# Performance work log

Measured on AMD Instinct MI355X. Metric: run time of the kernel, lower is better.

## Reference

```python
import math
import jax, jax.numpy as jnp
import numpy as np

B, S, E = 4, 2048, 768
H, D = 12, 64
LOCAL_H, GLOBAL_H = 8, 4
WINDOW_BASE, MIN_W, MAX_W = 128, 32, 512
GLOBAL_RATIO = 0.1
MASK_VALUE = -1e9


def setup_inputs() -> dict:
    key = jax.random.key(0)
    k1, k2, k3 = jax.random.split(key, 3)
    return {
        "x": jax.random.normal(k1, (B, S, E), dtype=jnp.float32),
        "w_attn": jax.random.normal(k2, (E, 3 * E), dtype=jnp.float32) * 0.02,
        "b_attn": jnp.zeros((3 * E,), dtype=jnp.float32),
        "w_proj": jax.random.normal(k3, (E, E), dtype=jnp.float32) * 0.02,
        "b_proj": jnp.zeros((E,), dtype=jnp.float32),
    }


def _masks(seq_len: int):
    # dynamic window (adaptive): base * sqrt(S/base), clamped
    w = int(WINDOW_BASE * math.sqrt(seq_len / WINDOW_BASE))
    w = max(MIN_W, min(w, MAX_W))
    half = w // 2
    i = jnp.arange(seq_len)[:, None]
    j = jnp.arange(seq_len)[None, :]
    # local: window band then causal override -> allowed iff i-half <= j <= i
    local_allowed = (j >= i - half) & (j <= i)
    local_mask = jnp.where(local_allowed, 0.0, MASK_VALUE).astype(jnp.float32)
    # global: columns at linspace positions allowed for all rows, plus full causal
    n_glob = max(1, int(seq_len * GLOBAL_RATIO))
    gpos = jnp.linspace(0.0, seq_len - 1, n_glob).astype(jnp.int32)
    is_gcol = jnp.zeros((seq_len,), dtype=bool).at[gpos].set(True)
    global_allowed = (j <= i) | is_gcol[None, :]
    global_mask = jnp.where(global_allowed, 0.0, MASK_VALUE).astype(jnp.float32)
    return local_mask, global_mask


def _attend(q, k, v, mask):
    # q,k,v: [B,h,S,D]; mask: [S,S]
    scale = 1.0 / math.sqrt(q.shape[-1])
    scores = jnp.einsum("bhqd,bhkd->bhqk", q, k) * scale + mask[None, None]
    w = jax.nn.softmax(scores, axis=-1)
    return jnp.einsum("bhqk,bhkd->bhqd", w, v)


def reference(x, w_attn, b_attn, w_proj, b_proj):
    b, s, _ = x.shape
    qkv = x @ w_attn + b_attn                       # [B,S,3E]
    q, k, v = jnp.split(qkv, 3, axis=-1)
    def heads(t):
        return t.reshape(b, s, H, D).transpose(0, 2, 1, 3)  # [B,H,S,D]
    q, k, v = heads(q), heads(k), heads(v)
    local_mask, global_mask = _masks(s)
    local_out = _attend(q[:, :LOCAL_H], k[:, :LOCAL_H], v[:, :LOCAL_H], local_mask)
    global_out = _attend(q[:, LOCAL_H:], k[:, LOCAL_H:], v[:, LOCAL_H:], global_mask)
    attn = jnp.concatenate([local_out, global_out], axis=1)  # heads 0..7 local, 8..11 global
    attn = attn.transpose(0, 2, 1, 3).reshape(b, s, E)
    return attn @ w_proj + b_proj
```

## Files before the change

kernel.cpp:

```cpp
#include <hip/hip_runtime.h>
#include <stdint.h>


#define NH 12
#define SQ 2048

typedef __bf16 bf16x8 __attribute__((ext_vector_type(8)));
typedef float f32x4 __attribute__((ext_vector_type(4)));

#define GLOAD_LDS16(g, l)                                                      \
  __builtin_amdgcn_global_load_lds(                                            \
      (__attribute__((address_space(1))) void*)(g),                            \
      (__attribute__((address_space(3))) void*)(l), 16, 0, 0)

__device__ __forceinline__ unsigned short bfbits(float f) {
  __bf16 h = (__bf16)f;
  return *(unsigned short*)&h;
}

__global__ __launch_bounds__(256) void prep(
    const float* __restrict__ x, unsigned short* __restrict__ xb,
    const float* __restrict__ w_attn, unsigned short* __restrict__ wattnT,
    const float* __restrict__ w_proj, unsigned short* __restrict__ wprojT) {
  const int bid = blockIdx.x, t = threadIdx.x;
  if (bid < 512) {
    const int n4 = 8192 * 768 / 4;
    for (int i = bid * 256 + t; i < n4; i += 512 * 256) {
      float4 v = ((const float4*)x)[i];
      ((ushort4*)xb)[i] = make_ushort4(bfbits(v.x), bfbits(v.y), bfbits(v.z), bfbits(v.w));
    }
    return;
  }
  __shared__ float tile[32][33];
  const float* in; unsigned short* out; int K, N, tl;
  if (bid < 512 + 72 * 24) { in = w_attn; out = wattnT; K = 768; N = 2304; tl = bid - 512; }
  else                     { in = w_proj; out = wprojT; K = 768; N = 768;  tl = bid - 512 - 72 * 24; }
  const int tpr = N / 32;
  const int n0 = (tl % tpr) * 32, k0 = (tl / tpr) * 32;
  const int tx = t & 31, ty = t >> 5;
  for (int r = ty; r < 32; r += 8) tile[r][tx] = in[(size_t)(k0 + r) * N + n0 + tx];
  __syncthreads();
  for (int r = ty; r < 32; r += 8) out[(size_t)(n0 + r) * K + k0 + tx] = bfbits(tile[tx][r]);
}

__global__ __launch_bounds__(256) void vprep(const unsigned short* __restrict__ QKV,
                                             const unsigned short* __restrict__ Vtb,
                                             unsigned short* __restrict__ Kg,
                                             unsigned short* __restrict__ VgT,
                                             int* __restrict__ gidx) {
  const int g = blockIdx.x, t = threadIdx.x;
  const int bh = g >> 3, y = g & 7;
  const int b = bh >> 2, h = 8 + (bh & 3);
  const int bh48 = b * NH + h;
  if (g == 0) {
    int c = t;
    gidx[c] = (c < 203) ? (int)((double)c * (2047.0 / 203.0)) : ((c == 203) ? 2047 : -1);
  }
  {
    int c = t, ch = y;
    int col = (c < 203) ? (int)((double)c * (2047.0 / 203.0)) : ((c == 203) ? 2047 : -1);
    uint4 v = {0u, 0u, 0u, 0u};
    if (col >= 0) v = *(const uint4*)&QKV[(size_t)(b * SQ + col) * 2304 + 768 + h * 64 + ch * 8];
    *(uint4*)&Kg[((size_t)bh * 256 + c) * 64 + ch * 8] = v;
  }
  {
    int d = t >> 2;
    int cb = (t & 3) * 64 + y * 8;
    for (int cc = 0; cc < 8; ++cc) {
      int c = cb + cc;
      int col = (c < 203) ? (int)((double)c * (2047.0 / 203.0)) : ((c == 203) ? 2047 : -1);
      unsigned short v = 0;
      if (col >= 0) v = Vtb[(size_t)bh48 * 131072 + (size_t)d * 2048 + col];
      VgT[((size_t)bh * 64 + d) * 256 + c] = v;
    }
  }
}

__device__ __forceinline__ void gemm_mainloop(
    const unsigned short* __restrict__ A, const unsigned short* __restrict__ BT,
    int m0, int n0, int tid,
    unsigned short* As, unsigned short* Bs,
    f32x4 acc[4][4]) {
  const int lane = tid & 63, wave = tid >> 6;
  const int wm = wave >> 1, wn = wave & 1;
  const int ln = lane & 15, quad = lane >> 4, ln7 = lane & 7;
  const int srow = tid >> 3;
  const int scol = ((tid & 7) ^ (srow & 7)) * 8;
  const int sbase = wave * 512;

#pragma unroll
  for (int mi = 0; mi < 4; ++mi)
#pragma unroll
    for (int ni = 0; ni < 4; ++ni) acc[mi][ni] = (f32x4){0.f, 0.f, 0.f, 0.f};

  auto stage = [&](int kt, int buf) {
    const int k0 = kt * 64;
    const int bo = buf * 8192;
#pragma unroll
    for (int rr = 0; rr < 4; ++rr) {
      GLOAD_LDS16(A  + (size_t)(m0 + rr * 32 + srow) * 768 + k0 + scol,
                  &As[bo + rr * 2048 + sbase]);
      GLOAD_LDS16(BT + (size_t)(n0 + rr * 32 + srow) * 768 + k0 + scol,
                  &Bs[bo + rr * 2048 + sbase]);
    }
  };

  stage(0, 0);
  int buf = 0;
  for (int kt = 0; kt < 12; ++kt) {
    if (kt < 11) {
      stage(kt + 1, buf ^ 1);
      asm volatile("s_waitcnt vmcnt(8)" ::: "memory");
    } else {
      asm volatile("s_waitcnt vmcnt(0)" ::: "memory");
    }
    __builtin_amdgcn_sched_barrier(0);
    __builtin_amdgcn_s_barrier();
    const int bo = buf * 8192;
#pragma unroll
    for (int kh = 0; kh < 2; ++kh) {
      const int sk = ((kh * 4 + quad) ^ ln7) * 8;
      bf16x8 aF[4], bF[4];
#pragma unroll
      for (int mi = 0; mi < 4; ++mi)
        aF[mi] = *(const bf16x8*)&As[bo + (wm * 64 + mi * 16 + ln) * 64 + sk];
#pragma unroll
      for (int ni = 0; ni < 4; ++ni)
        bF[ni] = *(const bf16x8*)&Bs[bo + (wn * 64 + ni * 16 + ln) * 64 + sk];
#pragma unroll
      for (int mi = 0; mi < 4; ++mi)
#pragma unroll
        for (int ni = 0; ni < 4; ++ni)
          acc[mi][ni] = __builtin_amdgcn_mfma_f32_16x16x32_bf16(aF[mi], bF[ni], acc[mi][ni], 0, 0, 0);
    }
    asm volatile("s_waitcnt lgkmcnt(0)" ::: "memory");
    __builtin_amdgcn_sched_barrier(0);
    __builtin_amdgcn_s_barrier();
    buf ^= 1;
  }
}

__global__ __launch_bounds__(256, 2) void qkv_gemm(
    const unsigned short* __restrict__ Xb, const unsigned short* __restrict__ WT,
    const float* __restrict__ bias, unsigned short* __restrict__ Out,
    unsigned short* __restrict__ Vtb) {
  __shared__ __attribute__((aligned(16))) unsigned short As[2 * 128 * 64];
  __shared__ __attribute__((aligned(16))) unsigned short Bs[2 * 128 * 64];
  f32x4 acc[4][4];
  const int wg = (blockIdx.x & 7) * 144 + (blockIdx.x >> 3);
  const int m0 = (wg / 18) * 128, n0 = (wg % 18) * 128;
  const int tid = threadIdx.x;
  gemm_mainloop(Xb, WT, m0, n0, tid, As, Bs, acc);
  const int lane = tid & 63, wave = tid >> 6;
  const int wm = wave >> 1, wn = wave & 1, ln = lane & 15, quad = lane >> 4;
  if (n0 < 1536) {
#pragma unroll
    for (int mi = 0; mi < 4; ++mi)
#pragma unroll
      for (int ni = 0; ni < 4; ++ni) {
        int n = n0 + wn * 64 + ni * 16 + ln;
        float bs = bias[n];
#pragma unroll
        for (int rg = 0; rg < 4; ++rg) {
          int m = m0 + wm * 64 + mi * 16 + quad * 4 + rg;
          Out[(size_t)m * 2304 + n] = bfbits(acc[mi][ni][rg] + bs);
        }
      }
  } else {
    const int bb = m0 >> 11;
    const int key0 = (m0 & 2047) + wm * 64;
#pragma unroll
    for (int ni = 0; ni < 4; ++ni) {
      int e = (n0 - 1536) + wn * 64 + ni * 16 + ln;
      int h = e >> 6, d = e & 63;
      float bs = bias[1536 + e];
      size_t rowb = (size_t)(bb * NH + h) * 131072 + (size_t)d * 2048;
#pragma unroll
      for (int mi = 0; mi < 4; ++mi) {
        int key = key0 + mi * 16 + quad * 4;
        unsigned int w0 = (unsigned int)bfbits(acc[mi][ni][0] + bs) |
                          ((unsigned int)bfbits(acc[mi][ni][1] + bs) << 16);
        unsigned int w1 = (unsigned int)bfbits(acc[mi][ni][2] + bs) |
                          ((unsigned int)bfbits(acc[mi][ni][3] + bs) << 16);
        *(unsigned int*)&Vtb[rowb + key]     = w0;
        *(unsigned int*)&Vtb[rowb + key + 2] = w1;
      }
    }
  }
}

__global__ __launch_bounds__(256, 2) void proj_gemm(
    const unsigned short* __restrict__ Ab, const unsigned short* __restrict__ WT,
    const float* __restrict__ bias, float* __restrict__ Out) {
  __shared__ __attribute__((aligned(16))) unsigned short As[2 * 128 * 64];
  __shared__ __attribute__((aligned(16))) unsigned short Bs[2 * 128 * 64];
  f32x4 acc[4][4];
  const int wg = (blockIdx.x & 7) * 48 + (blockIdx.x >> 3);
  const int m0 = (wg / 6) * 128, n0 = (wg % 6) * 128;
  const int tid = threadIdx.x;
  gemm_mainloop(Ab, WT, m0, n0, tid, As, Bs, acc);
  const int lane = tid & 63, wave = tid >> 6;
  const int wm = wave >> 1, wn = wave & 1, ln = lane & 15, quad = lane >> 4;
#pragma unroll
  for (int mi = 0; mi < 4; ++mi)
#pragma unroll
    for (int ni = 0; ni < 4; ++ni)
#pragma unroll
      for (int rg = 0; rg < 4; ++rg) {
        int m = m0 + wm * 64 + mi * 16 + quad * 4 + rg;
        int n = n0 + wn * 64 + ni * 16 + ln;
        Out[(size_t)m * 768 + n] = acc[mi][ni][rg] + bias[n];
      }
}

__global__ __launch_bounds__(256, 4) void attn_kernel(
    const unsigned short* __restrict__ QKV,
    const unsigned short* __restrict__ Vtb,
    const unsigned short* __restrict__ Kg, const unsigned short* __restrict__ VgT,
    const int* __restrict__ gidx,
    unsigned short* __restrict__ AOut,
    unsigned short* __restrict__ Opart,
    float* __restrict__ Lpart) {
  __shared__ __attribute__((aligned(16))) unsigned short Ks[64 * 64];
  __shared__ __attribute__((aligned(16))) unsigned short Vs[64 * 64];
  __shared__ __attribute__((aligned(16))) unsigned short Ps[64 * 64];

  const int gid = blockIdx.x;
  int b, h, qb, vt0, vt1;
  bool multi = false;
  if (gid < 1536) {
    int bh = gid / 96, rem = gid % 96;
    b = bh >> 2; h = 8 + (bh & 3);
    int part;
    if (rem < 4)       { qb = rem;                               part = 0; }
    else if (rem < 20) { int z = rem - 4;  qb = 4 + (z >> 1);    part = z & 1; }
    else if (rem < 44) { int z = rem - 20; int q = z / 3; qb = 12 + q; part = z - 3 * q; }
    else if (rem < 76) { int z = rem - 44; qb = 20 + (z >> 2);   part = z & 3; }
    else               { int z = rem - 76; int q = z / 5; qb = 28 + q; part = z - 5 * q; }
    vt0 = part * 8;
    vt1 = min(vt0 + 8, qb + 5);
    multi = (qb >= 4);
  } else {
    int lid = gid - 1536;
    int bh = lid >> 5; b = bh >> 3; h = bh & 7; qb = lid & 31;
    vt0 = ((qb > 4) ? qb - 4 : 0) + 4;
    vt1 = qb + 5;
  }
  const int qb0 = qb * 64;
  const bool is_local = (h < 8);
  const int tid = threadIdx.x, lane = tid & 63, wave = tid >> 6;
  const int ln = lane & 15, quad = lane >> 4;
  const int bh48 = b * NH + h;
  const int bhg = (b << 2) | (h & 3);

  const size_t qoff = (size_t)(b * SQ + qb0 + wave * 16 + ln) * 2304 + h * 64;
  bf16x8 qA0 = *(const bf16x8*)&QKV[qoff + quad * 8];
  bf16x8 qA1 = *(const bf16x8*)&QKV[qoff + 32 + quad * 8];

  bf16x8 onesF;
#pragma unroll
  for (int z = 0; z < 8; ++z) onesF[z] = (__bf16)1.0f;

  f32x4 o[4];
  f32x4 ls = (f32x4){0.f, 0.f, 0.f, 0.f};
#pragma unroll
  for (int dt = 0; dt < 4; ++dt) o[dt] = (f32x4){0.f, 0.f, 0.f, 0.f};

  const int irow = qb0 + wave * 16 + quad * 4;
  const int iw = qb0 + wave * 16;
  const int sr = tid >> 3, sch = tid & 7;
  const int ssw = (sch ^ (sr & 7)) * 8;
  const int s0k = (quad ^ (ln & 7)) * 8;
  const int s1k = ((quad + 4) ^ (ln & 7)) * 8;
  const int lnh = ln >> 3, ln7 = ln & 7;

  const float S2 = 0.125f * 1.44269504f, B2 = 8.0f * 1.44269504f;

  uint4 pk0, pk1, pv0, pv1;
  auto issue_load = [&](int vt) {
    if (vt >= 4) {
      const int kstart = (vt - 4) * 64;
      const size_t ko = (size_t)(b * SQ + kstart + sr) * 2304 + 768 + h * 64 + sch * 8;
      pk0 = *(const uint4*)&QKV[ko];
      pk1 = *(const uint4*)&QKV[ko + (size_t)32 * 2304];
      const size_t vo = (size_t)bh48 * 131072 + (size_t)sr * 2048 + kstart + sch * 8;
      pv0 = *(const uint4*)&Vtb[vo];
      pv1 = *(const uint4*)&Vtb[vo + 32 * 2048];
    } else {
      const int kg0 = vt * 64;
      pk0 = *(const uint4*)&Kg[((size_t)bhg * 256 + kg0 + sr) * 64 + sch * 8];
      pk1 = *(const uint4*)&Kg[((size_t)bhg * 256 + kg0 + 32 + sr) * 64 + sch * 8];
      pv0 = *(const uint4*)&VgT[((size_t)bhg * 64 + sr) * 256 + kg0 + sch * 8];
      pv1 = *(const uint4*)&VgT[((size_t)bhg * 64 + 32 + sr) * 256 + kg0 + sch * 8];
    }
  };
  issue_load(vt0);

  for (int vt = vt0; vt < vt1; ++vt) {
    const bool gph = (vt < 4);
    __syncthreads();
    *(uint4*)&Ks[sr * 64 + ssw]        = pk0;
    *(uint4*)&Ks[(32 + sr) * 64 + ssw] = pk1;
    *(uint4*)&Vs[sr * 64 + ssw]        = pv0;
    *(uint4*)&Vs[(32 + sr) * 64 + ssw] = pv1;
    __syncthreads();
    if (vt + 1 < vt1) issue_load(vt + 1);

    const int kstart = (vt - 4) * 64;
    const int kg0 = vt * 64;
    float sc[4][4];
    const bool full = !gph && (kstart + 63 <= iw) && (!is_local || kstart >= iw - 241);
#pragma unroll
    for (int nt = 0; nt < 4; ++nt) {
      bf16x8 kF0 = *(const bf16x8*)&Ks[(nt * 16 + ln) * 64 + s0k];
      bf16x8 kF1 = *(const bf16x8*)&Ks[(nt * 16 + ln) * 64 + s1k];
      f32x4 c = (f32x4){0.f, 0.f, 0.f, 0.f};
      c = __builtin_amdgcn_mfma_f32_16x16x32_bf16(qA0, kF0, c, 0, 0, 0);
      c = __builtin_amdgcn_mfma_f32_16x16x32_bf16(qA1, kF1, c, 0, 0, 0);
      if (full) {
#pragma unroll
        for (int rg = 0; rg < 4; ++rg) sc[nt][rg] = c[rg] * S2 - B2;
      } else if (!gph) {
        int j = kstart + nt * 16 + ln;
#pragma unroll
        for (int rg = 0; rg < 4; ++rg) {
          int i = irow + rg;
          bool ok = is_local ? (j >= i - 256 && j <= i) : (j <= i);
          sc[nt][rg] = ok ? (c[rg] * S2 - B2) : -1e9f;
        }
      } else {
        int jg = gidx[kg0 + nt * 16 + ln];
#pragma unroll
        for (int rg = 0; rg < 4; ++rg) {
          bool ok = jg > (irow + rg);
          sc[nt][rg] = ok ? (c[rg] * S2 - B2) : -1e9f;
        }
      }
    }

    __bf16* P = (__bf16*)Ps;
#pragma unroll
    for (int rg = 0; rg < 4; ++rg) {
      int prow = wave * 16 + quad * 4 + rg;
      int pbase = prow * 64 + ln7;
      int pr7 = prow & 7;
#pragma unroll
      for (int nt = 0; nt < 4; ++nt)
        P[pbase + (((nt * 2 + lnh) ^ pr7) << 3)] = (__bf16)exp2f(sc[nt][rg]);
    }
    bf16x8 pF0 = *(const bf16x8*)&Ps[(wave * 16 + ln) * 64 + s0k];
    bf16x8 pF1 = *(const bf16x8*)&Ps[(wave * 16 + ln) * 64 + s1k];
    ls = __builtin_amdgcn_mfma_f32_16x16x32_bf16(pF0, onesF, ls, 0, 0, 0);
    ls = __builtin_amdgcn_mfma_f32_16x16x32_bf16(pF1, onesF, ls, 0, 0, 0);
#pragma unroll
    for (int dt = 0; dt < 4; ++dt) {
      bf16x8 vF0 = *(const bf16x8*)&Vs[(dt * 16 + ln) * 64 + s0k];
      bf16x8 vF1 = *(const bf16x8*)&Vs[(dt * 16 + ln) * 64 + s1k];
      o[dt] = __builtin_amdgcn_mfma_f32_16x16x32_bf16(pF0, vF0, o[dt], 0, 0, 0);
      o[dt] = __builtin_amdgcn_mfma_f32_16x16x32_bf16(pF1, vF1, o[dt], 0, 0, 0);
    }
  }

  if (gid >= 1536 || !multi) {
#pragma unroll
    for (int dt = 0; dt < 4; ++dt)
#pragma unroll
      for (int rg = 0; rg < 4; ++rg) {
        int row = b * SQ + qb0 + wave * 16 + quad * 4 + rg;
        int e = h * 64 + dt * 16 + ln;
        AOut[(size_t)row * 768 + e] = bfbits(o[dt][rg] / ls[rg]);
      }
  } else {
#pragma unroll
    for (int dt = 0; dt < 4; ++dt)
#pragma unroll
      for (int rg = 0; rg < 4; ++rg) {
        int row = wave * 16 + quad * 4 + rg;
        Opart[(size_t)gid * 4096 + row * 64 + dt * 16 + ln] = bfbits(o[dt][rg]);
      }
    if (ln == 0) {
#pragma unroll
      for (int rg = 0; rg < 4; ++rg)
        Lpart[(size_t)gid * 64 + wave * 16 + quad * 4 + rg] = ls[rg];
    }
  }
}

__global__ __launch_bounds__(256) void combine_parts(
    const unsigned short* __restrict__ Opart, const float* __restrict__ Lpart,
    unsigned short* __restrict__ AOut) {
  const int bid = blockIdx.x;
  const int bh = bid / 28, qb = bid % 28 + 4;
  const int b = bh >> 2, h = 8 + (bh & 3);
  int C, np;
  if (qb < 12)      { C = 2 * qb - 4;  np = 2; }
  else if (qb < 20) { C = 3 * qb - 16; np = 3; }
  else if (qb < 28) { C = 4 * qb - 36; np = 4; }
  else              { C = 5 * qb - 64; np = 5; }
  const int slot0 = bh * 96 + C;
  const int t = threadIdx.x, r = t >> 2, c0 = (t & 3) * 16;
  float acc[16];
#pragma unroll
  for (int z = 0; z < 16; ++z) acc[z] = 0.f;
  float l = 0.f;
  for (int p = 0; p < np; ++p) {
    const unsigned short* src = &Opart[(size_t)(slot0 + p) * 4096 + r * 64 + c0];
    bf16x8 v0 = *(const bf16x8*)&src[0];
    bf16x8 v1 = *(const bf16x8*)&src[8];
#pragma unroll
    for (int z = 0; z < 8; ++z) { acc[z] += (float)v0[z]; acc[8 + z] += (float)v1[z]; }
    l += Lpart[(size_t)(slot0 + p) * 64 + r];
  }
  float inv = 1.f / l;
  unsigned short pk[16];
#pragma unroll
  for (int z = 0; z < 16; ++z) pk[z] = bfbits(acc[z] * inv);
  size_t dst = (size_t)(b * SQ + qb * 64 + r) * 768 + h * 64 + c0;
  *(uint4*)&AOut[dst]     = *(uint4*)&pk[0];
  *(uint4*)&AOut[dst + 8] = *(uint4*)&pk[8];
}

extern "C" void kernel_launch(void* const* d_in, const int* in_sizes, int n_in,
                              void* d_out, int out_size, void* d_ws, size_t ws_size,
                              hipStream_t stream) {
  const float* x      = (const float*)d_in[0];
  const float* w_attn = (const float*)d_in[1];
  const float* b_attn = (const float*)d_in[2];
  const float* w_proj = (const float*)d_in[3];
  const float* b_proj = (const float*)d_in[4];
  float* out = (float*)d_out;

  char* ws = (char*)d_ws;
  size_t off = 0;
  auto alloc = [&](size_t bytes) {
    void* p = ws + off;
    off += (bytes + 255) & ~(size_t)255;
    return p;
  };
  unsigned short* xb     = (unsigned short*)alloc((size_t)8192 * 768 * 2);
  unsigned short* wattnT = (unsigned short*)alloc((size_t)2304 * 768 * 2);
  unsigned short* wprojT = (unsigned short*)alloc((size_t)768 * 768 * 2);
  unsigned short* qkvb   = (unsigned short*)alloc((size_t)8192 * 2304 * 2);
  unsigned short* Vtb    = (unsigned short*)alloc((size_t)48 * 64 * 2048 * 2);
  unsigned short* Kgb    = (unsigned short*)alloc((size_t)16 * 256 * 64 * 2);
  unsigned short* VgTb   = (unsigned short*)alloc((size_t)16 * 64 * 256 * 2);
  int* gidxb             = (int*)alloc((size_t)256 * 4);
  unsigned short* Opartb = (unsigned short*)alloc((size_t)1536 * 4096 * 2);
  float* Lpartb          = (float*)alloc((size_t)1536 * 64 * 4);
  unsigned short* attnb  = xb;

  prep<<<dim3(512 + 72 * 24 + 24 * 24), dim3(256), 0, stream>>>(
      x, xb, w_attn, wattnT, w_proj, wprojT);
  qkv_gemm<<<dim3(1152), dim3(256), 0, stream>>>(xb, wattnT, b_attn, qkvb, Vtb);
  vprep<<<dim3(128), dim3(256), 0, stream>>>(qkvb, Vtb, Kgb, VgTb, gidxb);
  attn_kernel<<<dim3(2560), dim3(256), 0, stream>>>(qkvb, Vtb, Kgb, VgTb, gidxb,
                                                    attnb, Opartb, Lpartb);
  combine_parts<<<dim3(448), dim3(256), 0, stream>>>(Opartb, Lpartb, attnb);
  proj_gemm<<<dim3(384), dim3(256), 0, stream>>>(attnb, wprojT, b_proj, out);
}
```

Baseline: 205.3 us.

## Use two waves per attention block, each owning 32 query rows

The attention kernel now launches 128 threads (2 waves) instead of 4. Each wave handles two 16-row query fragments, so every K/V fragment read from shared memory feeds two MFMA row tiles. Each thread also stages twice as many K/V chunks per tile. This halves the LDS fragment reads per query row and the per-block thread count, at the cost of more registers per thread and fewer waves available to hide latency. The launch bounds change to (128, 2).

```diff
diff --git a/kernel.cpp b/kernel.cpp
--- a/kernel.cpp
+++ b/kernel.cpp
@@ -213,7 +213,7 @@
       }
 }
 
-__global__ __launch_bounds__(256, 4) void attn_kernel(
+__global__ __launch_bounds__(128, 2) void attn_kernel(
     const unsigned short* __restrict__ QKV,
     const unsigned short* __restrict__ Vtb,
     const unsigned short* __restrict__ Kg, const unsigned short* __restrict__ VgT,
@@ -253,21 +253,27 @@
   const int bh48 = b * NH + h;
   const int bhg = (b << 2) | (h & 3);
 
-  const size_t qoff = (size_t)(b * SQ + qb0 + wave * 16 + ln) * 2304 + h * 64;
-  bf16x8 qA0 = *(const bf16x8*)&QKV[qoff + quad * 8];
-  bf16x8 qA1 = *(const bf16x8*)&QKV[qoff + 32 + quad * 8];
+  bf16x8 qA[2][2];
+#pragma unroll
+  for (int mf = 0; mf < 2; ++mf) {
+    const size_t qoff = (size_t)(b * SQ + qb0 + wave * 32 + mf * 16 + ln) * 2304 + h * 64;
+    qA[mf][0] = *(const bf16x8*)&QKV[qoff + quad * 8];
+    qA[mf][1] = *(const bf16x8*)&QKV[qoff + 32 + quad * 8];
+  }
 
   bf16x8 onesF;
 #pragma unroll
   for (int z = 0; z < 8; ++z) onesF[z] = (__bf16)1.0f;
 
-  f32x4 o[4];
-  f32x4 ls = (f32x4){0.f, 0.f, 0.f, 0.f};
-#pragma unroll
-  for (int dt = 0; dt < 4; ++dt) o[dt] = (f32x4){0.f, 0.f, 0.f, 0.f};
-
-  const int irow = qb0 + wave * 16 + quad * 4;
-  const int iw = qb0 + wave * 16;
+  f32x4 o[2][4];
+  f32x4 ls[2];
+#pragma unroll
+  for (int mf = 0; mf < 2; ++mf) {
+    ls[mf] = (f32x4){0.f, 0.f, 0.f, 0.f};
+#pragma unroll
+    for (int dt = 0; dt < 4; ++dt) o[mf][dt] = (f32x4){0.f, 0.f, 0.f, 0.f};
+  }
+
   const int sr = tid >> 3, sch = tid & 7;
   const int ssw = (sch ^ (sr & 7)) * 8;
   const int s0k = (quad ^ (ln & 7)) * 8;
@@ -276,22 +282,22 @@
 
   const float S2 = 0.125f * 1.44269504f, B2 = 8.0f * 1.44269504f;
 
-  uint4 pk0, pk1, pv0, pv1;
+  uint4 pk[4], pv[4];
   auto issue_load = [&](int vt) {
     if (vt >= 4) {
       const int kstart = (vt - 4) * 64;
-      const size_t ko = (size_t)(b * SQ + kstart + sr) * 2304 + 768 + h * 64 + sch * 8;
-      pk0 = *(const uint4*)&QKV[ko];
-      pk1 = *(const uint4*)&QKV[ko + (size_t)32 * 2304];
-      const size_t vo = (size_t)bh48 * 131072 + (size_t)sr * 2048 + kstart + sch * 8;
-      pv0 = *(const uint4*)&Vtb[vo];
-      pv1 = *(const uint4*)&Vtb[vo + 32 * 2048];
+#pragma unroll
+      for (int i = 0; i < 4; ++i) {
+        pk[i] = *(const uint4*)&QKV[(size_t)(b * SQ + kstart + sr + 16 * i) * 2304 + 768 + h * 64 + sch * 8];
+        pv[i] = *(const uint4*)&Vtb[(size_t)bh48 * 131072 + (size_t)(sr + 16 * i) * 2048 + kstart + sch * 8];
+      }
     } else {
       const int kg0 = vt * 64;
-      pk0 = *(const uint4*)&Kg[((size_t)bhg * 256 + kg0 + sr) * 64 + sch * 8];
-      pk1 = *(const uint4*)&Kg[((size_t)bhg * 256 + kg0 + 32 + sr) * 64 + sch * 8];
-      pv0 = *(const uint4*)&VgT[((size_t)bhg * 64 + sr) * 256 + kg0 + sch * 8];
-      pv1 = *(const uint4*)&VgT[((size_t)bhg * 64 + 32 + sr) * 256 + kg0 + sch * 8];
+#pragma unroll
+      for (int i = 0; i < 4; ++i) {
+        pk[i] = *(const uint4*)&Kg[((size_t)bhg * 256 + kg0 + sr + 16 * i) * 64 + sch * 8];
+        pv[i] = *(const uint4*)&VgT[((size_t)bhg * 64 + sr + 16 * i) * 256 + kg0 + sch * 8];
+      }
     }
   };
   issue_load(vt0);
@@ -299,89 +305,109 @@
   for (int vt = vt0; vt < vt1; ++vt) {
     const bool gph = (vt < 4);
     __syncthreads();
-    *(uint4*)&Ks[sr * 64 + ssw]        = pk0;
-    *(uint4*)&Ks[(32 + sr) * 64 + ssw] = pk1;
-    *(uint4*)&Vs[sr * 64 + ssw]        = pv0;
-    *(uint4*)&Vs[(32 + sr) * 64 + ssw] = pv1;
+#pragma unroll
+    for (int i = 0; i < 4; ++i) {
+      *(uint4*)&Ks[(sr + 16 * i) * 64 + ssw] = pk[i];
+      *(uint4*)&Vs[(sr + 16 * i) * 64 + ssw] = pv[i];
+    }
     __syncthreads();
     if (vt + 1 < vt1) issue_load(vt + 1);
 
     const int kstart = (vt - 4) * 64;
     const int kg0 = vt * 64;
-    float sc[4][4];
-    const bool full = !gph && (kstart + 63 <= iw) && (!is_local || kstart >= iw - 241);
+    bool fullm[2];
+#pragma unroll
+    for (int mf = 0; mf < 2; ++mf) {
+      int iw = qb0 + wave * 32 + mf * 16;
+      fullm[mf] = !gph && (kstart + 63 <= iw) && (!is_local || kstart >= iw - 241);
+    }
+
+    __bf16* P = (__bf16*)Ps;
 #pragma unroll
     for (int nt = 0; nt < 4; ++nt) {
       bf16x8 kF0 = *(const bf16x8*)&Ks[(nt * 16 + ln) * 64 + s0k];
       bf16x8 kF1 = *(const bf16x8*)&Ks[(nt * 16 + ln) * 64 + s1k];
-      f32x4 c = (f32x4){0.f, 0.f, 0.f, 0.f};
-      c = __builtin_amdgcn_mfma_f32_16x16x32_bf16(qA0, kF0, c, 0, 0, 0);
-      c = __builtin_amdgcn_mfma_f32_16x16x32_bf16(qA1, kF1, c, 0, 0, 0);
-      if (full) {
-#pragma unroll
-        for (int rg = 0; rg < 4; ++rg) sc[nt][rg] = c[rg] * S2 - B2;
-      } else if (!gph) {
-        int j = kstart + nt * 16 + ln;
+#pragma unroll
+      for (int mf = 0; mf < 2; ++mf) {
+        f32x4 c = (f32x4){0.f, 0.f, 0.f, 0.f};
+        c = __builtin_amdgcn_mfma_f32_16x16x32_bf16(qA[mf][0], kF0, c, 0, 0, 0);
+        c = __builtin_amdgcn_mfma_f32_16x16x32_bf16(qA[mf][1], kF1, c, 0, 0, 0);
+        const int irow = qb0 + wave * 32 + mf * 16 + quad * 4;
+        float sc[4];
+        if (fullm[mf]) {
+#pragma unroll
+          for (int rg = 0; rg < 4; ++rg) sc[rg] = c[rg] * S2 - B2;
+        } else if (!gph) {
+          int j = kstart + nt * 16 + ln;
+#pragma unroll
+          for (int rg = 0; rg < 4; ++rg) {
+            int i = irow + rg;
+            bool ok = is_local ? (j >= i - 256 && j <= i) : (j <= i);
+            sc[rg] = ok ? (c[rg] * S2 - B2) : -1e9f;
+          }
+        } else {
+          int jg = gidx[kg0 + nt * 16 + ln];
+#pragma unroll
+          for (int rg = 0; rg < 4; ++rg) {
+            bool ok = jg > (irow + rg);
+            sc[rg] = ok ? (c[rg] * S2 - B2) : -1e9f;
+          }
+        }
 #pragma unroll
         for (int rg = 0; rg < 4; ++rg) {
-          int i = irow + rg;
-          bool ok = is_local ? (j >= i - 256 && j <= i) : (j <= i);
-          sc[nt][rg] = ok ? (c[rg] * S2 - B2) : -1e9f;
+          int prow = wave * 32 + mf * 16 + quad * 4 + rg;
+          P[prow * 64 + ln7 + (((nt * 2 + lnh) ^ (prow & 7)) << 3)] = (__bf16)exp2f(sc[rg]);
         }
-      } else {
-        int jg = gidx[kg0 + nt * 16 + ln];
-#pragma unroll
-        for (int rg = 0; rg < 4; ++rg) {
-          bool ok = jg > (irow + rg);
-          sc[nt][rg] = ok ? (c[rg] * S2 - B2) : -1e9f;
-        }
-      }
-    }
-
-    __bf16* P = (__bf16*)Ps;
-#pragma unroll
-    for (int rg = 0; rg < 4; ++rg) {
-      int prow = wave * 16 + quad * 4 + rg;
-      int pbase = prow * 64 + ln7;
-      int pr7 = prow & 7;
-#pragma unroll
-      for (int nt = 0; nt < 4; ++nt)
-        P[pbase + (((nt * 2 + lnh) ^ pr7) << 3)] = (__bf16)exp2f(sc[nt][rg]);
-    }
-    bf16x8 pF0 = *(const bf16x8*)&Ps[(wave * 16 + ln) * 64 + s0k];
-    bf16x8 pF1 = *(const bf16x8*)&Ps[(wave * 16 + ln) * 64 + s1k];
-    ls = __builtin_amdgcn_mfma_f32_16x16x32_bf16(pF0, onesF, ls, 0, 0, 0);
-    ls = __builtin_amdgcn_mfma_f32_16x16x32_bf16(pF1, onesF, ls, 0, 0, 0);
+      }
+    }
+
+    bf16x8 pF[2][2];
+#pragma unroll
+    for (int mf = 0; mf < 2; ++mf) {
+      pF[mf][0] = *(const bf16x8*)&Ps[(wave * 32 + mf * 16 + ln) * 64 + s0k];
+      pF[mf][1] = *(const bf16x8*)&Ps[(wave * 32 + mf * 16 + ln) * 64 + s1k];
+      ls[mf] = __builtin_amdgcn_mfma_f32_16x16x32_bf16(pF[mf][0], onesF, ls[mf], 0, 0, 0);
+      ls[mf] = __builtin_amdgcn_mfma_f32_16x16x32_bf16(pF[mf][1], onesF, ls[mf], 0, 0, 0);
+    }
 #pragma unroll
     for (int dt = 0; dt < 4; ++dt) {
       bf16x8 vF0 = *(const bf16x8*)&Vs[(dt * 16 + ln) * 64 + s0k];
       bf16x8 vF1 = *(const bf16x8*)&Vs[(dt * 16 + ln) * 64 + s1k];
-      o[dt] = __builtin_amdgcn_mfma_f32_16x16x32_bf16(pF0, vF0, o[dt], 0, 0, 0);
-      o[dt] = __builtin_amdgcn_mfma_f32_16x16x32_bf16(pF1, vF1, o[dt], 0, 0, 0);
+#pragma unroll
+      for (int mf = 0; mf < 2; ++mf) {
+        o[mf][dt] = __builtin_amdgcn_mfma_f32_16x16x32_bf16(pF[mf][0], vF0, o[mf][dt], 0, 0, 0);
+        o[mf][dt] = __builtin_amdgcn_mfma_f32_16x16x32_bf16(pF[mf][1], vF1, o[mf][dt], 0, 0, 0);
+      }
     }
   }
 
   if (gid >= 1536 || !multi) {
 #pragma unroll
-    for (int dt = 0; dt < 4; ++dt)
-#pragma unroll
-      for (int rg = 0; rg < 4; ++rg) {
-        int row = b * SQ + qb0 + wave * 16 + quad * 4 + rg;
-        int e = h * 64 + dt * 16 + ln;
-        AOut[(size_t)row * 768 + e] = bfbits(o[dt][rg] / ls[rg]);
-      }
+    for (int mf = 0; mf < 2; ++mf)
+#pragma unroll
+      for (int dt = 0; dt < 4; ++dt)
+#pragma unroll
+        for (int rg = 0; rg < 4; ++rg) {
+          int row = b * SQ + qb0 + wave * 32 + mf * 16 + quad * 4 + rg;
+          int e = h * 64 + dt * 16 + ln;
+          AOut[(size_t)row * 768 + e] = bfbits(o[mf][dt][rg] / ls[mf][rg]);
+        }
   } else {
 #pragma unroll
-    for (int dt = 0; dt < 4; ++dt)
-#pragma unroll
-      for (int rg = 0; rg < 4; ++rg) {
-        int row = wave * 16 + quad * 4 + rg;
-        Opart[(size_t)gid * 4096 + row * 64 + dt * 16 + ln] = bfbits(o[dt][rg]);
-      }
+    for (int mf = 0; mf < 2; ++mf)
+#pragma unroll
+      for (int dt = 0; dt < 4; ++dt)
+#pragma unroll
+        for (int rg = 0; rg < 4; ++rg) {
+          int row = wave * 32 + mf * 16 + quad * 4 + rg;
+          Opart[(size_t)gid * 4096 + row * 64 + dt * 16 + ln] = bfbits(o[mf][dt][rg]);
+        }
     if (ln == 0) {
 #pragma unroll
-      for (int rg = 0; rg < 4; ++rg)
-        Lpart[(size_t)gid * 64 + wave * 16 + quad * 4 + rg] = ls[rg];
+      for (int mf = 0; mf < 2; ++mf)
+#pragma unroll
+        for (int rg = 0; rg < 4; ++rg)
+          Lpart[(size_t)gid * 64 + wave * 32 + mf * 16 + quad * 4 + rg] = ls[mf][rg];
     }
   }
 }
@@ -453,7 +479,7 @@
       x, xb, w_attn, wattnT, w_proj, wprojT);
   qkv_gemm<<<dim3(1152), dim3(256), 0, stream>>>(xb, wattnT, b_attn, qkvb, Vtb);
   vprep<<<dim3(128), dim3(256), 0, stream>>>(qkvb, Vtb, Kgb, VgTb, gidxb);
-  attn_kernel<<<dim3(2560), dim3(256), 0, stream>>>(qkvb, Vtb, Kgb, VgTb, gidxb,
+  attn_kernel<<<dim3(2560), dim3(128), 0, stream>>>(qkvb, Vtb, Kgb, VgTb, gidxb,
                                                     attnb, Opartb, Lpartb);
   combine_parts<<<dim3(448), dim3(256), 0, stream>>>(Opartb, Lpartb, attnb);
   proj_gemm<<<dim3(384), dim3(256), 0, stream>>>(attnb, wprojT, b_proj, out);
```

After: 304.6 us. 1.48x slower.

## Double-buffer K/V tiles in LDS with direct global-to-LDS async loads

Applied to the files above, without the earlier changes.

Replaces the register-staged K/V loads with global_load_lds direct-to-LDS copies into two ping-pong LDS buffers. The next tile is prefetched while the current one is computed, synchronised with explicit vmcnt/lgkmcnt waits and raw barriers. This removes the VGPR round trip and the LDS store instructions, at the cost of twice the LDS for K/V, which may reduce occupancy at the requested 4 blocks per SM. The swizzle is now applied on the global source side, and correctness depends on the hand-written waitcnt counts.

```diff
diff --git a/kernel.cpp b/kernel.cpp
--- a/kernel.cpp
+++ b/kernel.cpp
@@ -221,8 +221,8 @@
     unsigned short* __restrict__ AOut,
     unsigned short* __restrict__ Opart,
     float* __restrict__ Lpart) {
-  __shared__ __attribute__((aligned(16))) unsigned short Ks[64 * 64];
-  __shared__ __attribute__((aligned(16))) unsigned short Vs[64 * 64];
+  __shared__ __attribute__((aligned(16))) unsigned short Ks[2][64 * 64];
+  __shared__ __attribute__((aligned(16))) unsigned short Vs[2][64 * 64];
   __shared__ __attribute__((aligned(16))) unsigned short Ps[64 * 64];
 
   const int gid = blockIdx.x;
@@ -268,43 +268,47 @@
 
   const int irow = qb0 + wave * 16 + quad * 4;
   const int iw = qb0 + wave * 16;
-  const int sr = tid >> 3, sch = tid & 7;
-  const int ssw = (sch ^ (sr & 7)) * 8;
   const int s0k = (quad ^ (ln & 7)) * 8;
   const int s1k = ((quad + 4) ^ (ln & 7)) * 8;
   const int lnh = ln >> 3, ln7 = ln & 7;
+  const int srw = lane >> 3;
+  const int scol = ((lane & 7) ^ srw) * 8;
 
   const float S2 = 0.125f * 1.44269504f, B2 = 8.0f * 1.44269504f;
 
-  uint4 pk0, pk1, pv0, pv1;
-  auto issue_load = [&](int vt) {
-    if (vt >= 4) {
-      const int kstart = (vt - 4) * 64;
-      const size_t ko = (size_t)(b * SQ + kstart + sr) * 2304 + 768 + h * 64 + sch * 8;
-      pk0 = *(const uint4*)&QKV[ko];
-      pk1 = *(const uint4*)&QKV[ko + (size_t)32 * 2304];
-      const size_t vo = (size_t)bh48 * 131072 + (size_t)sr * 2048 + kstart + sch * 8;
-      pv0 = *(const uint4*)&Vtb[vo];
-      pv1 = *(const uint4*)&Vtb[vo + 32 * 2048];
-    } else {
-      const int kg0 = vt * 64;
-      pk0 = *(const uint4*)&Kg[((size_t)bhg * 256 + kg0 + sr) * 64 + sch * 8];
-      pk1 = *(const uint4*)&Kg[((size_t)bhg * 256 + kg0 + 32 + sr) * 64 + sch * 8];
-      pv0 = *(const uint4*)&VgT[((size_t)bhg * 64 + sr) * 256 + kg0 + sch * 8];
-      pv1 = *(const uint4*)&VgT[((size_t)bhg * 64 + 32 + sr) * 256 + kg0 + sch * 8];
+  auto stage = [&](int vt, int bufsel) {
+#pragma unroll
+    for (int p = 0; p < 2; ++p) {
+      const int r0 = (wave * 2 + p) * 8;
+      const int ldso = (wave * 2 + p) * 512;
+      if (vt >= 4) {
+        const int kstart = (vt - 4) * 64;
+        GLOAD_LDS16(QKV + (size_t)(b * SQ + kstart + r0 + srw) * 2304 + 768 + h * 64 + scol,
+                    &Ks[bufsel][ldso]);
+        GLOAD_LDS16(Vtb + (size_t)bh48 * 131072 + (size_t)(r0 + srw) * 2048 + kstart + scol,
+                    &Vs[bufsel][ldso]);
+      } else {
+        const int kg0 = vt * 64;
+        GLOAD_LDS16(Kg  + ((size_t)bhg * 256 + kg0 + r0 + srw) * 64 + scol,
+                    &Ks[bufsel][ldso]);
+        GLOAD_LDS16(VgT + ((size_t)bhg * 64 + r0 + srw) * 256 + kg0 + scol,
+                    &Vs[bufsel][ldso]);
+      }
     }
   };
-  issue_load(vt0);
-
+
+  stage(vt0, 0);
+  int buf = 0;
   for (int vt = vt0; vt < vt1; ++vt) {
     const bool gph = (vt < 4);
-    __syncthreads();
-    *(uint4*)&Ks[sr * 64 + ssw]        = pk0;
-    *(uint4*)&Ks[(32 + sr) * 64 + ssw] = pk1;
-    *(uint4*)&Vs[sr * 64 + ssw]        = pv0;
-    *(uint4*)&Vs[(32 + sr) * 64 + ssw] = pv1;
-    __syncthreads();
-    if (vt + 1 < vt1) issue_load(vt + 1);
+    if (vt + 1 < vt1) {
+      stage(vt + 1, buf ^ 1);
+      asm volatile("s_waitcnt vmcnt(4)" ::: "memory");
+    } else {
+      asm volatile("s_waitcnt vmcnt(0)" ::: "memory");
+    }
+    __builtin_amdgcn_sched_barrier(0);
+    __builtin_amdgcn_s_barrier();
 
     const int kstart = (vt - 4) * 64;
     const int kg0 = vt * 64;
@@ -312,8 +316,8 @@
     const bool full = !gph && (kstart + 63 <= iw) && (!is_local || kstart >= iw - 241);
 #pragma unroll
     for (int nt = 0; nt < 4; ++nt) {
-      bf16x8 kF0 = *(const bf16x8*)&Ks[(nt * 16 + ln) * 64 + s0k];
-      bf16x8 kF1 = *(const bf16x8*)&Ks[(nt * 16 + ln) * 64 + s1k];
+      bf16x8 kF0 = *(const bf16x8*)&Ks[buf][(nt * 16 + ln) * 64 + s0k];
+      bf16x8 kF1 = *(const bf16x8*)&Ks[buf][(nt * 16 + ln) * 64 + s1k];
       f32x4 c = (f32x4){0.f, 0.f, 0.f, 0.f};
       c = __builtin_amdgcn_mfma_f32_16x16x32_bf16(qA0, kF0, c, 0, 0, 0);
       c = __builtin_amdgcn_mfma_f32_16x16x32_bf16(qA1, kF1, c, 0, 0, 0);
@@ -354,11 +358,16 @@
     ls = __builtin_amdgcn_mfma_f32_16x16x32_bf16(pF1, onesF, ls, 0, 0, 0);
 #pragma unroll
     for (int dt = 0; dt < 4; ++dt) {
-      bf16x8 vF0 = *(const bf16x8*)&Vs[(dt * 16 + ln) * 64 + s0k];
-      bf16x8 vF1 = *(const bf16x8*)&Vs[(dt * 16 + ln) * 64 + s1k];
+      bf16x8 vF0 = *(const bf16x8*)&Vs[buf][(dt * 16 + ln) * 64 + s0k];
+      bf16x8 vF1 = *(const bf16x8*)&Vs[buf][(dt * 16 + ln) * 64 + s1k];
       o[dt] = __builtin_amdgcn_mfma_f32_16x16x32_bf16(pF0, vF0, o[dt], 0, 0, 0);
       o[dt] = __builtin_amdgcn_mfma_f32_16x16x32_bf16(pF1, vF1, o[dt], 0, 0, 0);
     }
+
+    asm volatile("s_waitcnt lgkmcnt(0)" ::: "memory");
+    __builtin_amdgcn_sched_barrier(0);
+    __builtin_amdgcn_s_barrier();
+    buf ^= 1;
   }
 
   if (gid >= 1536 || !multi) {
```

After: 207.6 us. No clear change (+1.1%).
